# Kernel tuning notes

Hardware: AMD Instinct MI355X
Metric: run time of the kernel (lower is better)

## Reference

```python
import jax, jax.numpy as jnp
import numpy as np
import math

H, Dh, S = 8, 64, 3          # heads, dim per head, samples factor
B, T, N, K = 2, 12, 512, 16  # batch, time, nodes, local-adj width
F = H * Dh                   # features = 512
SN = int(S * math.log2(N))   # Sampled_Nodes = 27
EPS = 1e-5


def setup_inputs() -> dict:
    key = jax.random.key(0)
    ks = jax.random.split(key, 22)
    sc = 1.0 / math.sqrt(F)
    W = lambda k: jax.random.normal(k, (F, F), jnp.float32) * sc
    bb = lambda k: jax.random.normal(k, (F,), jnp.float32) * 0.01
    return {
        "x": jax.random.normal(ks[0], (B, T, N, F), jnp.float32),
        "spa_eigvalue": jax.random.normal(ks[1], (F,), jnp.float32) * 0.1,
        "spa_eigvec": jax.random.normal(ks[2], (N, F), jnp.float32) * 0.1,
        "tem_eigvalue": jax.random.normal(ks[3], (F,), jnp.float32) * 0.1,
        "tem_eigvec": jax.random.normal(ks[4], (N, F), jnp.float32) * 0.1,
        "localadj": jax.random.randint(ks[5], (N, K), 0, N),
        "Wq": W(ks[6]), "bq": bb(ks[7]),
        "Wk": W(ks[8]), "bk": bb(ks[9]),
        "Wv": W(ks[10]), "bv": bb(ks[11]),
        "Wo": W(ks[12]), "bo": bb(ks[13]),
        "w_proj": jax.random.normal(ks[14], (K,), jnp.float32) / math.sqrt(K),
        "b_proj": jax.random.normal(ks[15], (), jnp.float32) * 0.01,
        "gamma": jnp.ones((F,), jnp.float32),
        "beta": jnp.zeros((F,), jnp.float32),
        "W1": W(ks[16]), "b1": bb(ks[17]),
        "W2": W(ks[18]), "b2": bb(ks[19]),
    }


def _lin(v, Wm, bv):  # torch nn.Linear: y = x @ W^T + b, W is [out, in]
    return jnp.einsum('...i,oi->...o', v, Wm) + bv


def _ln(v, g=None, b=None):  # LayerNorm over last dim, eps=1e-5
    mu = jnp.mean(v, -1, keepdims=True)
    var = jnp.var(v, -1, keepdims=True)
    y = (v - mu) * jax.lax.rsqrt(var + EPS)
    return y * g + b if g is not None else y


def reference(x, spa_eigvalue, spa_eigvec, tem_eigvalue, tem_eigvec, localadj,
              Wq, bq, Wk, bk, Wv, bv, Wo, bo, w_proj, b_proj,
              gamma, beta, W1, b1, W2, b2):
    # eigvec @ diag(eigval) == row-wise scaling
    x_ = x + (spa_eigvec * spa_eigvalue + tem_eigvec * tem_eigvalue)
    to_heads = lambda v: v.reshape(B, T, N, H, Dh).transpose(3, 0, 1, 2, 4)  # [H,B,T,N,Dh]
    Qh = to_heads(_lin(x_, Wq, bq))
    Kh = to_heads(_lin(x_, Wk, bk))
    Vh = to_heads(_lin(x_, Wv, bv))
    # local-adjacency K sampling: [H,B,T,N,K,Dh]
    Ks = Kh[:, :, :, localadj, :]
    qks = jnp.einsum('hbtnd,hbtnkd->hbtnk', Qh, Ks)
    # importance score per query node via learned projection over K neighbors
    M = jnp.einsum('hbtnk,k->hbtn', qks, w_proj) + b_proj
    _, m_top = jax.lax.top_k(M, SN)                              # [H,B,T,SN]
    Qr = jnp.take_along_axis(Qh, m_top[..., None], axis=3)       # [H,B,T,SN,Dh]
    scores = jnp.einsum('hbtsd,hbtnd->hbtsn', Qr, Kh) / math.sqrt(Dh)
    attn = jax.nn.softmax(scores, axis=-1)                       # [H,B,T,SN,N]
    cp = jnp.argmax(attn, axis=-2)                               # best sampled query per key node [H,B,T,N]
    val = jnp.einsum('hbtsn,hbtnd->hbtsd', attn, Vh)             # [H,B,T,SN,Dh]
    out = jnp.take_along_axis(val, cp[..., None], axis=3)        # [H,B,T,N,Dh]
    out = out.transpose(1, 2, 3, 0, 4).reshape(B, T, N, F)       # merge heads
    v = _ln(_lin(out, Wo, bo), gamma, beta)
    h = jax.nn.relu(_lin(v, W1, b1))
    h = _lin(h, W2, b2) + v
    return _ln(h)
```

## Files before the change

kernel.cpp:

```cpp
#include <hip/hip_runtime.h>
#include <math.h>

#define H_    8
#define DH    64
#define NN    512
#define KADJ  16
#define FF    512
#define BTOT  24
#define ROWS  12288
#define SN_   27
#define EPS_  1e-5f

typedef short short8 __attribute__((ext_vector_type(8)));
typedef float f32x4  __attribute__((ext_vector_type(4)));

__device__ __forceinline__ ushort f2bf(float x) {
    uint u = __float_as_uint(x);
    u += 0x7FFFu + ((u >> 16) & 1u);
    return (ushort)(u >> 16);
}
__device__ __forceinline__ float bf2f(ushort h) {
    return __uint_as_float(((uint)h) << 16);
}

__device__ __forceinline__ void gload_lds16(const ushort* g, ushort* l) {
    __builtin_amdgcn_global_load_lds(
        (const __attribute__((address_space(1))) unsigned int*)g,
        (__attribute__((address_space(3))) unsigned int*)l,
        16, 0, 0);
}

__global__ __launch_bounds__(256) void add_pos_bf16(
    const float* __restrict__ x,
    const float* __restrict__ spa_val, const float* __restrict__ spa_vec,
    const float* __restrict__ tem_val, const float* __restrict__ tem_vec,
    ushort* __restrict__ xh, ushort* __restrict__ xl)
{
    int i = blockIdx.x * 256 + threadIdx.x;
    int f4  = i & 127;
    int row = i >> 7;
    int n   = row & (NN - 1);

    float4 xv = reinterpret_cast<const float4*>(x)[i];
    float4 sv = reinterpret_cast<const float4*>(spa_vec)[n * 128 + f4];
    float4 tv = reinterpret_cast<const float4*>(tem_vec)[n * 128 + f4];
    float4 se = reinterpret_cast<const float4*>(spa_val)[f4];
    float4 te = reinterpret_cast<const float4*>(tem_val)[f4];
    float r0 = xv.x + sv.x * se.x + tv.x * te.x;
    float r1 = xv.y + sv.y * se.y + tv.y * te.y;
    float r2 = xv.z + sv.z * se.z + tv.z * te.z;
    float r3 = xv.w + sv.w * se.w + tv.w * te.w;
    ushort h0 = f2bf(r0), h1 = f2bf(r1), h2 = f2bf(r2), h3 = f2bf(r3);
    reinterpret_cast<ushort4*>(xh)[i] = make_ushort4(h0, h1, h2, h3);
    reinterpret_cast<ushort4*>(xl)[i] = make_ushort4(
        f2bf(r0 - bf2f(h0)), f2bf(r1 - bf2f(h1)),
        f2bf(r2 - bf2f(h2)), f2bf(r3 - bf2f(h3)));
}

__global__ __launch_bounds__(256) void wconv_kernel(
    const float* __restrict__ w0, const float* __restrict__ w1,
    const float* __restrict__ w2, const float* __restrict__ w3,
    const float* __restrict__ w4, const float* __restrict__ w5,
    ushort* __restrict__ whi, ushort* __restrict__ wlo)
{
    const int wi = blockIdx.y;
    const float* W = wi == 0 ? w0 : wi == 1 ? w1 : wi == 2 ? w2 :
                     wi == 3 ? w3 : wi == 4 ? w4 : w5;
    int i = blockIdx.x * 256 + threadIdx.x;
    float4 v = reinterpret_cast<const float4*>(W)[i];
    ushort h0 = f2bf(v.x), h1 = f2bf(v.y), h2 = f2bf(v.z), h3 = f2bf(v.w);
    reinterpret_cast<ushort4*>(whi + (size_t)wi * 262144)[i] =
        make_ushort4(h0, h1, h2, h3);
    if (wi < 2) {
        reinterpret_cast<ushort4*>(wlo + (size_t)wi * 262144)[i] =
            make_ushort4(f2bf(v.x - bf2f(h0)), f2bf(v.y - bf2f(h1)),
                         f2bf(v.z - bf2f(h2)), f2bf(v.w - bf2f(h3)));
    }
}

#define GBM 64
#define GBN 128

__global__ __launch_bounds__(256, 2) void gemm_qk(
    const ushort* __restrict__ Axh, long aLo,
    const ushort* __restrict__ Wh0, long wLo, long wK,
    const float* __restrict__ bq, const float* __restrict__ bk,
    ushort* __restrict__ Qh, ushort* __restrict__ Ql,
    ushort* __restrict__ Kh, ushort* __restrict__ Kl)
{
    __shared__ ushort sAh[GBM * 64];
    __shared__ ushort sAl[GBM * 64];
    __shared__ ushort sBh[2][GBN * 64];
    __shared__ ushort sBl[2][GBN * 64];

    const int nx  = gridDim.x >> 3;
    const int bid = blockIdx.x;
    const int lt  = (bid & 7) * nx + (bid >> 3);
    const int rowBase = (lt >> 2) * GBM;
    const int colBase = (lt & 3) * GBN;

    const int tid  = threadIdx.x;
    const int lane = tid & 63;
    const int wid  = tid >> 6;
    const int q    = lane >> 4;
    const int fr   = lane & 15;
    const int wm   = wid & 1;
    const int wn   = wid >> 1;

    const ushort* asrc[2];
    const ushort* bsrc[4];
    #pragma unroll
    for (int c = 0; c < 2; ++c) {
        const int p   = wid * 2048 + c * 1024 + lane * 16;
        const int row = p >> 7;
        const int ss  = ((p >> 4) & 7) ^ (row & 7);
        asrc[c] = Axh + (size_t)(rowBase + row) * FF + ss * 8;
    }
    #pragma unroll
    for (int c = 0; c < 4; ++c) {
        const int p   = wid * 4096 + c * 1024 + lane * 16;
        const int row = p >> 7;
        const int ss  = ((p >> 4) & 7) ^ (row & 7);
        bsrc[c] = Wh0 + (size_t)(colBase + row) * FF + ss * 8;
    }

    f32x4 accQ[2][4], accK[2][4];
    #pragma unroll
    for (int mi = 0; mi < 2; ++mi)
        #pragma unroll
        for (int ni = 0; ni < 4; ++ni) {
            accQ[mi][ni] = (f32x4){0.f, 0.f, 0.f, 0.f};
            accK[mi][ni] = (f32x4){0.f, 0.f, 0.f, 0.f};
        }

    const int swz = fr & 7;

    for (int step = 0; step < 8; ++step) {
        #pragma unroll
        for (int c = 0; c < 2; ++c) {
            gload_lds16(asrc[c],       &sAh[wid * 1024 + c * 512]);
            gload_lds16(asrc[c] + aLo, &sAl[wid * 1024 + c * 512]);
            asrc[c] += 64;
        }
        #pragma unroll
        for (int c = 0; c < 4; ++c) {
            gload_lds16(bsrc[c],            &sBh[0][wid * 2048 + c * 512]);
            gload_lds16(bsrc[c] + wLo,      &sBl[0][wid * 2048 + c * 512]);
            gload_lds16(bsrc[c] + wK,       &sBh[1][wid * 2048 + c * 512]);
            gload_lds16(bsrc[c] + wK + wLo, &sBl[1][wid * 2048 + c * 512]);
            bsrc[c] += 64;
        }
        __syncthreads();

        #pragma unroll
        for (int ksub = 0; ksub < 2; ++ksub) {
            const int kq = (ksub * 4 + q) ^ swz;
            short8 ah[2], al[2];
            #pragma unroll
            for (int mi = 0; mi < 2; ++mi) {
                ah[mi] = *(const short8*)&sAh[(wm * 32 + mi * 16 + fr) * 64 + (kq << 3)];
                al[mi] = *(const short8*)&sAl[(wm * 32 + mi * 16 + fr) * 64 + (kq << 3)];
            }
            __builtin_amdgcn_s_setprio(1);
            #pragma unroll
            for (int qk = 0; qk < 2; ++qk) {
                short8 bh[4], bl[4];
                #pragma unroll
                for (int ni = 0; ni < 4; ++ni) {
                    bh[ni] = *(const short8*)&sBh[qk][(wn * 64 + ni * 16 + fr) * 64 + (kq << 3)];
                    bl[ni] = *(const short8*)&sBl[qk][(wn * 64 + ni * 16 + fr) * 64 + (kq << 3)];
                }
                f32x4 (*acc)[4] = qk == 0 ? accQ : accK;
                #pragma unroll
                for (int mi = 0; mi < 2; ++mi)
                    #pragma unroll
                    for (int ni = 0; ni < 4; ++ni)
                        acc[mi][ni] = __builtin_amdgcn_mfma_f32_16x16x32_bf16(
                            ah[mi], bh[ni], acc[mi][ni], 0, 0, 0);
                #pragma unroll
                for (int mi = 0; mi < 2; ++mi)
                    #pragma unroll
                    for (int ni = 0; ni < 4; ++ni)
                        acc[mi][ni] = __builtin_amdgcn_mfma_f32_16x16x32_bf16(
                            ah[mi], bl[ni], acc[mi][ni], 0, 0, 0);
                #pragma unroll
                for (int mi = 0; mi < 2; ++mi)
                    #pragma unroll
                    for (int ni = 0; ni < 4; ++ni)
                        acc[mi][ni] = __builtin_amdgcn_mfma_f32_16x16x32_bf16(
                            al[mi], bh[ni], acc[mi][ni], 0, 0, 0);
            }
            __builtin_amdgcn_s_setprio(0);
        }
        __syncthreads();
    }

    #pragma unroll
    for (int mi = 0; mi < 2; ++mi)
        #pragma unroll
        for (int ni = 0; ni < 4; ++ni) {
            const int col = colBase + wn * 64 + ni * 16 + fr;
            const float bqc = bq[col];
            const float bkc = bk[col];
            #pragma unroll
            for (int r = 0; r < 4; ++r) {
                const int row = rowBase + wm * 32 + mi * 16 + q * 4 + r;
                const size_t idx = (size_t)row * FF + col;
                float vq = accQ[mi][ni][r] + bqc;
                ushort hq = f2bf(vq);
                Qh[idx] = hq;
                Ql[idx] = f2bf(vq - bf2f(hq));
                float vk = accK[mi][ni][r] + bkc;
                ushort hk = f2bf(vk);
                Kh[idx] = hk;
                Kl[idx] = f2bf(vk - bf2f(hk));
            }
        }
}

template <int EPI, int OUT>
__global__ __launch_bounds__(256, 2) void gemm_mfma2(
    const ushort* __restrict__ Ah, const ushort* __restrict__ Wh,
    const float* __restrict__ bias, const float* __restrict__ addsrc,
    float* __restrict__ Cf, ushort* __restrict__ Cb)
{
    __shared__ ushort sA[GBM * 128];
    __shared__ ushort sB[GBN * 128];

    const int nx  = gridDim.x >> 3;
    const int bid = blockIdx.x;
    const int lt  = (bid & 7) * nx + (bid >> 3);
    const int rowBase = (lt >> 2) * GBM;
    const int colBase = (lt & 3) * GBN;

    const int tid  = threadIdx.x;
    const int lane = tid & 63;
    const int wid  = tid >> 6;
    const int q    = lane >> 4;
    const int fr   = lane & 15;
    const int wm   = wid & 1;
    const int wn   = wid >> 1;

    const ushort* asrc[4];
    const ushort* bsrc[8];
    #pragma unroll
    for (int c = 0; c < 4; ++c) {
        const int p   = wid * 4096 + c * 1024 + lane * 16;
        const int row = p >> 8;
        const int ss  = ((p >> 4) & 15) ^ (row & 7);
        asrc[c] = Ah + (size_t)(rowBase + row) * FF + ss * 8;
    }
    #pragma unroll
    for (int c = 0; c < 8; ++c) {
        const int p   = wid * 8192 + c * 1024 + lane * 16;
        const int row = p >> 8;
        const int ss  = ((p >> 4) & 15) ^ (row & 7);
        bsrc[c] = Wh + (size_t)(colBase + row) * FF + ss * 8;
    }

    f32x4 acc[2][4];
    #pragma unroll
    for (int mi = 0; mi < 2; ++mi)
        #pragma unroll
        for (int ni = 0; ni < 4; ++ni) acc[mi][ni] = (f32x4){0.f, 0.f, 0.f, 0.f};

    const int swz = fr & 7;

    for (int step = 0; step < 4; ++step) {
        #pragma unroll
        for (int c = 0; c < 4; ++c) {
            gload_lds16(asrc[c], &sA[wid * 2048 + c * 512]);
            asrc[c] += 128;
        }
        #pragma unroll
        for (int c = 0; c < 8; ++c) {
            gload_lds16(bsrc[c], &sB[wid * 4096 + c * 512]);
            bsrc[c] += 128;
        }
        __syncthreads();

        #pragma unroll
        for (int ksub = 0; ksub < 4; ++ksub) {
            const int kq = (ksub * 4 + q) ^ swz;
            short8 af[2], bf[4];
            #pragma unroll
            for (int mi = 0; mi < 2; ++mi)
                af[mi] = *(const short8*)&sA[(wm * 32 + mi * 16 + fr) * 128 + (kq << 3)];
            #pragma unroll
            for (int ni = 0; ni < 4; ++ni)
                bf[ni] = *(const short8*)&sB[(wn * 64 + ni * 16 + fr) * 128 + (kq << 3)];
            #pragma unroll
            for (int mi = 0; mi < 2; ++mi)
                #pragma unroll
                for (int ni = 0; ni < 4; ++ni)
                    acc[mi][ni] = __builtin_amdgcn_mfma_f32_16x16x32_bf16(
                        af[mi], bf[ni], acc[mi][ni], 0, 0, 0);
        }
        __syncthreads();
    }

    #pragma unroll
    for (int mi = 0; mi < 2; ++mi)
        #pragma unroll
        for (int ni = 0; ni < 4; ++ni) {
            const int col = colBase + wn * 64 + ni * 16 + fr;
            const float bcol = bias[col];
            #pragma unroll
            for (int r = 0; r < 4; ++r) {
                const int row = rowBase + wm * 32 + mi * 16 + q * 4 + r;
                float v = acc[mi][ni][r] + bcol;
                if (EPI == 1) v = fmaxf(v, 0.0f);
                if (EPI == 2) v += addsrc[(size_t)row * FF + col];
                const size_t idx = (size_t)row * FF + col;
                if (OUT == 0) Cf[idx] = v;
                if (OUT == 1) Cb[idx] = f2bf(v);
            }
        }
}

__global__ __launch_bounds__(256) void qks_M_kernel(
    const ushort* __restrict__ Qh, const ushort* __restrict__ Ql,
    const ushort* __restrict__ Kh, const ushort* __restrict__ Kl,
    const int* __restrict__ adj, const float* __restrict__ w_proj,
    const float* __restrict__ b_proj, float* __restrict__ Mout)
{
    const int unit = blockIdx.x * 16 + (threadIdx.x >> 4);
    const int l16  = threadIdx.x & 15;
    const int n    = unit & (NN - 1);
    const int hbt  = unit >> 9;
    const int h    = hbt / BTOT;
    const int bt   = hbt - h * BTOT;

    const uint headbase = (uint)(bt * NN) * FF + h * DH + l16 * 4;
    const ushort* khB = Kh + headbase;
    const ushort* klB = Kl + headbase;

    const int   aj = adj[n * KADJ + l16];
    f32x4 acc = (f32x4){0.f, 0.f, 0.f, 0.f};

    #pragma unroll
    for (int k = 0; k < KADJ; ++k) {
        const int  j   = __shfl(aj, k, 16);
        const float wk = w_proj[k];
        const uint off = (uint)j * FF;
        uint2 hu = *(const uint2*)(khB + off);
        uint2 lu = *(const uint2*)(klB + off);
        float k0 = __uint_as_float(hu.x << 16) + __uint_as_float(lu.x << 16);
        float k1 = __uint_as_float(hu.x & 0xFFFF0000u) +
                   __uint_as_float(lu.x & 0xFFFF0000u);
        float k2 = __uint_as_float(hu.y << 16) + __uint_as_float(lu.y << 16);
        float k3 = __uint_as_float(hu.y & 0xFFFF0000u) +
                   __uint_as_float(lu.y & 0xFFFF0000u);
        acc[0] += wk * k0; acc[1] += wk * k1;
        acc[2] += wk * k2; acc[3] += wk * k3;
    }

    const uint qidx = headbase + (uint)n * FF;
    uint2 qhu = *(const uint2*)(Qh + qidx);
    uint2 qlu = *(const uint2*)(Ql + qidx);
    float q0 = __uint_as_float(qhu.x << 16) + __uint_as_float(qlu.x << 16);
    float q1 = __uint_as_float(qhu.x & 0xFFFF0000u) +
               __uint_as_float(qlu.x & 0xFFFF0000u);
    float q2 = __uint_as_float(qhu.y << 16) + __uint_as_float(qlu.y << 16);
    float q3 = __uint_as_float(qhu.y & 0xFFFF0000u) +
               __uint_as_float(qlu.y & 0xFFFF0000u);
    float t = q0 * acc[0] + q1 * acc[1] + q2 * acc[2] + q3 * acc[3];
    #pragma unroll
    for (int o = 1; o <= 8; o <<= 1) t += __shfl_xor(t, o);
    if (l16 == 0) Mout[unit] = t + b_proj[0];
}

__global__ __launch_bounds__(512) void topk_kernel(
    const float* __restrict__ M, int* __restrict__ mtop)
{
    __shared__ float vals[NN];
    const int g = blockIdx.x;
    const int n = threadIdx.x;
    const float m = M[(size_t)g * NN + n];
    vals[n] = m;
    __syncthreads();

    int cnt = 0;
    #pragma unroll 16
    for (int j = 0; j < NN; ++j) {
        const float vj = vals[j];
        cnt += (vj > m || (vj == m && j < n)) ? 1 : 0;
    }
    if (cnt < SN_) mtop[g * SN_ + cnt] = n;
}

__global__ __launch_bounds__(1024) void fused_attn(
    const ushort* __restrict__ Qh, const ushort* __restrict__ Ql,
    const ushort* __restrict__ Kh, const ushort* __restrict__ Kl,
    const ushort* __restrict__ Vb, const int* __restrict__ mtop,
    ushort* __restrict__ attnout)
{
    __shared__ ushort P_lds[32 * 512];
    __shared__ ushort Vt_lds[64 * 512];
    __shared__ float red0[16][32];
    __shared__ float red1[16][32];
    __shared__ float val2[2][32][68];
    __shared__ int   cp_lds[NN];
    __shared__ int   mt[32];

    const int g = blockIdx.x;
    const int h = g / BTOT, bt = g % BTOT;
    const int tid = threadIdx.x;
    const int wave = tid >> 6, lane = tid & 63;
    const int q = lane >> 4, c = lane & 15;
    const size_t base_bt = (size_t)bt * NN * FF;
    const int hcol = h * DH;

    if (tid < 32) mt[tid] = mtop[g * SN_ + (tid < SN_ ? tid : 0)];
    __syncthreads();

    const int n0 = wave * 32;
    short8 bfh[2][2], bfl[2][2];
    #pragma unroll
    for (int nt = 0; nt < 2; ++nt) {
        const size_t kp = base_bt + (size_t)(n0 + nt * 16 + c) * FF + hcol + q * 8;
        #pragma unroll
        for (int ks = 0; ks < 2; ++ks) {
            bfh[nt][ks] = *(const short8*)&Kh[kp + ks * 32];
            bfl[nt][ks] = *(const short8*)&Kl[kp + ks * 32];
        }
    }

    ushort4 vreg[2][4];
    #pragma unroll
    for (int i = 0; i < 2; ++i) {
        const int u  = tid + i * 1024;
        const int d4 = u & 15, ng = u >> 4;
        #pragma unroll
        for (int ii = 0; ii < 4; ++ii)
            vreg[i][ii] = *(const ushort4*)&Vb[base_bt +
                (size_t)(ng * 4 + ii) * FF + hcol + d4 * 4];
    }

    short8 afh[2][2], afl[2][2];
    #pragma unroll
    for (int m = 0; m < 2; ++m) {
        const int grow = mt[m * 16 + c];
        const size_t qp = base_bt + (size_t)grow * FF + hcol + q * 8;
        #pragma unroll
        for (int ks = 0; ks < 2; ++ks) {
            afh[m][ks] = *(const short8*)&Qh[qp + ks * 32];
            afl[m][ks] = *(const short8*)&Ql[qp + ks * 32];
        }
    }

    f32x4 sc[2][2];
    #pragma unroll
    for (int m = 0; m < 2; ++m)
        #pragma unroll
        for (int nt = 0; nt < 2; ++nt) sc[m][nt] = (f32x4){0.f, 0.f, 0.f, 0.f};
    __builtin_amdgcn_s_setprio(1);
    #pragma unroll
    for (int ks = 0; ks < 2; ++ks)
        #pragma unroll
        for (int m = 0; m < 2; ++m)
            #pragma unroll
            for (int nt = 0; nt < 2; ++nt) {
                sc[m][nt] = __builtin_amdgcn_mfma_f32_16x16x32_bf16(
                    afh[m][ks], bfh[nt][ks], sc[m][nt], 0, 0, 0);
                sc[m][nt] = __builtin_amdgcn_mfma_f32_16x16x32_bf16(
                    afh[m][ks], bfl[nt][ks], sc[m][nt], 0, 0, 0);
                sc[m][nt] = __builtin_amdgcn_mfma_f32_16x16x32_bf16(
                    afl[m][ks], bfh[nt][ks], sc[m][nt], 0, 0, 0);
            }
    __builtin_amdgcn_s_setprio(0);
    #pragma unroll
    for (int m = 0; m < 2; ++m)
        #pragma unroll
        for (int nt = 0; nt < 2; ++nt)
            #pragma unroll
            for (int r = 0; r < 4; ++r) sc[m][nt][r] *= 0.125f;

    float rmax[2][4];
    #pragma unroll
    for (int m = 0; m < 2; ++m)
        #pragma unroll
        for (int r = 0; r < 4; ++r)
            rmax[m][r] = fmaxf(sc[m][0][r], sc[m][1][r]);
    #pragma unroll
    for (int off = 1; off <= 8; off <<= 1)
        #pragma unroll
        for (int m = 0; m < 2; ++m)
            #pragma unroll
            for (int r = 0; r < 4; ++r)
                rmax[m][r] = fmaxf(rmax[m][r], __shfl_xor(rmax[m][r], off));
    if (c == 0) {
        #pragma unroll
        for (int m = 0; m < 2; ++m)
            #pragma unroll
            for (int r = 0; r < 4; ++r)
                red0[wave][m * 16 + q * 4 + r] = rmax[m][r];
    }
    __syncthreads();
    float gmax[2][4];
    #pragma unroll
    for (int m = 0; m < 2; ++m)
        #pragma unroll
        for (int r = 0; r < 4; ++r) {
            const int row = m * 16 + q * 4 + r;
            float v = red0[0][row];
            #pragma unroll
            for (int w = 1; w < 16; ++w) v = fmaxf(v, red0[w][row]);
            gmax[m][r] = v;
        }

    float rsum[2][4] = {};
    #pragma unroll
    for (int m = 0; m < 2; ++m)
        #pragma unroll
        for (int nt = 0; nt < 2; ++nt)
            #pragma unroll
            for (int r = 0; r < 4; ++r) {
                float e = expf(sc[m][nt][r] - gmax[m][r]);
                sc[m][nt][r] = e;
                rsum[m][r] += e;
            }
    #pragma unroll
    for (int off = 1; off <= 8; off <<= 1)
        #pragma unroll
        for (int m = 0; m < 2; ++m)
            #pragma unroll
            for (int r = 0; r < 4; ++r)
                rsum[m][r] += __shfl_xor(rsum[m][r], off);
    if (c == 0) {
        #pragma unroll
        for (int m = 0; m < 2; ++m)
            #pragma unroll
            for (int r = 0; r < 4; ++r)
                red1[wave][m * 16 + q * 4 + r] = rsum[m][r];
    }
    __syncthreads();
    #pragma unroll
    for (int m = 0; m < 2; ++m)
        #pragma unroll
        for (int r = 0; r < 4; ++r) {
            const int row = m * 16 + q * 4 + r;
            float s = red1[0][row];
            #pragma unroll
            for (int w = 1; w < 16; ++w) s += red1[w][row];
            const float inv = 1.0f / s;
            #pragma unroll
            for (int nt = 0; nt < 2; ++nt) sc[m][nt][r] *= inv;
        }

    #pragma unroll
    for (int nt = 0; nt < 2; ++nt) {
        float bv = -INFINITY;
        int bi = 1 << 30;
        #pragma unroll
        for (int m = 0; m < 2; ++m)
            #pragma unroll
            for (int r = 0; r < 4; ++r) {
                const int row = m * 16 + q * 4 + r;
                if (row < SN_) {
                    float v = sc[m][nt][r];
                    if (v > bv) { bv = v; bi = row; }
                }
            }
        #pragma unroll
        for (int off = 16; off <= 32; off <<= 1) {
            float ov = __shfl_xor(bv, off);
            int   oi = __shfl_xor(bi, off);
            if (ov > bv || (ov == bv && oi < bi)) { bv = ov; bi = oi; }
        }
        if (q == 0) cp_lds[n0 + nt * 16 + c] = bi;
    }

    #pragma unroll
    for (int m = 0; m < 2; ++m)
        #pragma unroll
        for (int nt = 0; nt < 2; ++nt)
            #pragma unroll
            for (int r = 0; r < 4; ++r) {
                const int row = m * 16 + q * 4 + r;
                const int col = n0 + nt * 16 + c;
                P_lds[(row * 512 + col) ^ ((row & 7) << 3)] = f2bf(sc[m][nt][r]);
            }

    #pragma unroll
    for (int i = 0; i < 2; ++i) {
        const int u  = tid + i * 1024;
        const int d4 = u & 15, ng = u >> 4;
        const int n0v = ng * 4;
        #pragma unroll
        for (int j = 0; j < 4; ++j) {
            const int d = d4 * 4 + j;
            ushort4 t;
            t.x = ((const ushort*)&vreg[i][0])[j];
            t.y = ((const ushort*)&vreg[i][1])[j];
            t.z = ((const ushort*)&vreg[i][2])[j];
            t.w = ((const ushort*)&vreg[i][3])[j];
            *(ushort4*)&Vt_lds[(d * 512 + n0v) ^ ((d & 7) << 3)] = t;
        }
    }
    __syncthreads();

    const int kh = wave >> 3, rem = wave & 7;
    const int msel = rem >> 2, dt = rem & 3;
    const int dcol = dt * 16 + c;
    const int prow = msel * 16 + c;
    const int pswz = (prow & 7) << 3;
    const int vswz = (dcol & 7) << 3;
    f32x4 acc = (f32x4){0.f, 0.f, 0.f, 0.f};
    __builtin_amdgcn_s_setprio(1);
    #pragma unroll
    for (int ks8 = 0; ks8 < 8; ++ks8) {
        const int kstep = kh * 8 + ks8;
        short8 a = *(const short8*)&P_lds[(prow * 512 + kstep * 32 + q * 8) ^ pswz];
        short8 b = *(const short8*)&Vt_lds[(dcol * 512 + kstep * 32 + q * 8) ^ vswz];
        acc = __builtin_amdgcn_mfma_f32_16x16x32_bf16(a, b, acc, 0, 0, 0);
    }
    __builtin_amdgcn_s_setprio(0);
    #pragma unroll
    for (int r = 0; r < 4; ++r)
        val2[kh][msel * 16 + q * 4 + r][dt * 16 + c] = acc[r];
    __syncthreads();

    #pragma unroll
    for (int pass = 0; pass < 4; ++pass) {
        const int n  = pass * 128 + (tid >> 3);
        const int s  = cp_lds[n];
        const int d0 = (tid & 7) * 8;
        float vr[8];
        #pragma unroll
        for (int j = 0; j < 8; ++j)
            vr[j] = val2[0][s][d0 + j] + val2[1][s][d0 + j];
        uint4 u;
        u.x = (uint)f2bf(vr[0]) | ((uint)f2bf(vr[1]) << 16);
        u.y = (uint)f2bf(vr[2]) | ((uint)f2bf(vr[3]) << 16);
        u.z = (uint)f2bf(vr[4]) | ((uint)f2bf(vr[5]) << 16);
        u.w = (uint)f2bf(vr[6]) | ((uint)f2bf(vr[7]) << 16);
        *(uint4*)(attnout + base_bt + (size_t)n * FF + hcol + d0) = u;
    }
}

template <int AFFINE, int BFOUT>
__global__ __launch_bounds__(256) void ln_kernel(
    const float* __restrict__ X, const float* __restrict__ g,
    const float* __restrict__ b, float* __restrict__ Yf,
    ushort* __restrict__ Yb, int rows)
{
    const int row = blockIdx.x * 4 + (threadIdx.x >> 6);
    if (row >= rows) return;
    const int lane = threadIdx.x & 63;
    const float4* x4 = reinterpret_cast<const float4*>(X + (size_t)row * FF);
    float4 a = x4[lane];
    float4 c = x4[lane + 64];
    float s = a.x + a.y + a.z + a.w + c.x + c.y + c.z + c.w;
    float q = a.x * a.x + a.y * a.y + a.z * a.z + a.w * a.w +
              c.x * c.x + c.y * c.y + c.z * c.z + c.w * c.w;
    #pragma unroll
    for (int o = 32; o; o >>= 1) {
        s += __shfl_xor(s, o);
        q += __shfl_xor(q, o);
    }
    const float mu   = s * (1.0f / FF);
    const float var  = q * (1.0f / FF) - mu * mu;
    const float rstd = 1.0f / sqrtf(var + EPS_);

    float4 ya, yc;
    ya.x = (a.x - mu) * rstd; ya.y = (a.y - mu) * rstd;
    ya.z = (a.z - mu) * rstd; ya.w = (a.w - mu) * rstd;
    yc.x = (c.x - mu) * rstd; yc.y = (c.y - mu) * rstd;
    yc.z = (c.z - mu) * rstd; yc.w = (c.w - mu) * rstd;
    if (AFFINE) {
        float4 ga = reinterpret_cast<const float4*>(g)[lane];
        float4 gc = reinterpret_cast<const float4*>(g)[lane + 64];
        float4 ba = reinterpret_cast<const float4*>(b)[lane];
        float4 bc = reinterpret_cast<const float4*>(b)[lane + 64];
        ya.x = ya.x * ga.x + ba.x; ya.y = ya.y * ga.y + ba.y;
        ya.z = ya.z * ga.z + ba.z; ya.w = ya.w * ga.w + ba.w;
        yc.x = yc.x * gc.x + bc.x; yc.y = yc.y * gc.y + bc.y;
        yc.z = yc.z * gc.z + bc.z; yc.w = yc.w * gc.w + bc.w;
    }
    float4* y4 = reinterpret_cast<float4*>(Yf + (size_t)row * FF);
    y4[lane]      = ya;
    y4[lane + 64] = yc;
    if (BFOUT) {
        ushort4* yb = reinterpret_cast<ushort4*>(Yb + (size_t)row * FF);
        yb[lane] = make_ushort4(f2bf(ya.x), f2bf(ya.y), f2bf(ya.z), f2bf(ya.w));
        yb[lane + 64] = make_ushort4(f2bf(yc.x), f2bf(yc.y), f2bf(yc.z), f2bf(yc.w));
    }
}

extern "C" void kernel_launch(void* const* d_in, const int* in_sizes, int n_in,
                              void* d_out, int out_size, void* d_ws, size_t ws_size,
                              hipStream_t stream)
{
    const float* x       = (const float*)d_in[0];
    const float* spa_val = (const float*)d_in[1];
    const float* spa_vec = (const float*)d_in[2];
    const float* tem_val = (const float*)d_in[3];
    const float* tem_vec = (const float*)d_in[4];
    const int*   adj     = (const int*)  d_in[5];
    const float* Wq = (const float*)d_in[6];  const float* bq = (const float*)d_in[7];
    const float* Wk = (const float*)d_in[8];  const float* bk = (const float*)d_in[9];
    const float* Wv = (const float*)d_in[10]; const float* bv = (const float*)d_in[11];
    const float* Wo = (const float*)d_in[12]; const float* bo = (const float*)d_in[13];
    const float* w_proj = (const float*)d_in[14];
    const float* b_proj = (const float*)d_in[15];
    const float* gamma  = (const float*)d_in[16];
    const float* beta   = (const float*)d_in[17];
    const float* W1 = (const float*)d_in[18]; const float* b1 = (const float*)d_in[19];
    const float* W2 = (const float*)d_in[20]; const float* b2 = (const float*)d_in[21];

    float* out = (float*)d_out;

    const size_t R = (size_t)ROWS * FF;

    ushort* ws_u = (ushort*)d_ws;
    ushort* bufQh = ws_u;
    ushort* bufQl = ws_u + R;
    ushort* bufKh = ws_u + 2 * R;
    ushort* bufKl = ws_u + 3 * R;
    ushort* bufVb = ws_u + 4 * R;
    ushort* whi   = ws_u + 5 * R;
    ushort* wlo   = whi + 6 * 262144;
    float*  Mbuf  = (float*)(wlo + 2 * 262144);
    int*    mtop  = (int*)(Mbuf + (size_t)H_ * BTOT * NN);

    float* o_f32 = (float*)bufQh;
    float* v_f32 = (float*)bufKh;
    float* h2_f32 = (float*)bufQh;

    ushort* xh  = (ushort*)d_out;
    ushort* xl  = xh + R;
    ushort* attnout = xh;
    ushort* vbf = xl;
    ushort* h1b = xh;

    add_pos_bf16<<<(ROWS * FF / 4) / 256, 256, 0, stream>>>(
        x, spa_val, spa_vec, tem_val, tem_vec, xh, xl);

    wconv_kernel<<<dim3(256, 6), 256, 0, stream>>>(Wq, Wk, Wv, Wo, W1, W2, whi, wlo);

    const int NG = (ROWS / GBM) * (FF / GBN);
    gemm_qk<<<NG, 256, 0, stream>>>(xh, (long)R,
                                    whi, (long)(6 * 262144), (long)262144,
                                    bq, bk, bufQh, bufQl, bufKh, bufKl);
    gemm_mfma2<0, 1><<<NG, 256, 0, stream>>>(xh, whi + 2 * 262144, bv, nullptr,
                                             nullptr, bufVb);

    qks_M_kernel<<<(H_ * BTOT * NN) / 16, 256, 0, stream>>>(
        bufQh, bufQl, bufKh, bufKl, adj, w_proj, b_proj, Mbuf);
    topk_kernel<<<H_ * BTOT, 512, 0, stream>>>(Mbuf, mtop);

    fused_attn<<<H_ * BTOT, 1024, 0, stream>>>(
        bufQh, bufQl, bufKh, bufKl, bufVb, mtop, attnout);

    gemm_mfma2<0, 0><<<NG, 256, 0, stream>>>(attnout, whi + 3 * 262144, bo, nullptr,
                                             o_f32, nullptr);
    ln_kernel<1, 1><<<ROWS / 4, 256, 0, stream>>>(o_f32, gamma, beta, v_f32, vbf, ROWS);
    gemm_mfma2<1, 1><<<NG, 256, 0, stream>>>(vbf, whi + 4 * 262144, b1, nullptr,
                                             nullptr, h1b);
    gemm_mfma2<2, 0><<<NG, 256, 0, stream>>>(h1b, whi + 5 * 262144, b2, v_f32,
                                             h2_f32, nullptr);
    ln_kernel<0, 0><<<ROWS / 4, 256, 0, stream>>>(h2_f32, nullptr, nullptr, out, nullptr, ROWS);
}
```

Before: 211.7 us.

## Store post-attention intermediates in bf16 and drop setprio in QK GEMM

```diff
diff --git a/kernel.cpp b/kernel.cpp
--- a/kernel.cpp
+++ b/kernel.cpp
@@ -161,7 +161,6 @@
                 ah[mi] = *(const short8*)&sAh[(wm * 32 + mi * 16 + fr) * 64 + (kq << 3)];
                 al[mi] = *(const short8*)&sAl[(wm * 32 + mi * 16 + fr) * 64 + (kq << 3)];
             }
-            __builtin_amdgcn_s_setprio(1);
             #pragma unroll
             for (int qk = 0; qk < 2; ++qk) {
                 short8 bh[4], bl[4];
@@ -190,7 +189,6 @@
                         acc[mi][ni] = __builtin_amdgcn_mfma_f32_16x16x32_bf16(
                             al[mi], bh[ni], acc[mi][ni], 0, 0, 0);
             }
-            __builtin_amdgcn_s_setprio(0);
         }
         __syncthreads();
     }
@@ -221,7 +219,7 @@
 template <int EPI, int OUT>
 __global__ __launch_bounds__(256, 2) void gemm_mfma2(
     const ushort* __restrict__ Ah, const ushort* __restrict__ Wh,
-    const float* __restrict__ bias, const float* __restrict__ addsrc,
+    const float* __restrict__ bias, const ushort* __restrict__ addsrc_bf,
     float* __restrict__ Cf, ushort* __restrict__ Cb)
 {
     __shared__ ushort sA[GBM * 128];
@@ -310,8 +308,8 @@
                 const int row = rowBase + wm * 32 + mi * 16 + q * 4 + r;
                 float v = acc[mi][ni][r] + bcol;
                 if (EPI == 1) v = fmaxf(v, 0.0f);
-                if (EPI == 2) v += addsrc[(size_t)row * FF + col];
                 const size_t idx = (size_t)row * FF + col;
+                if (EPI == 2) v += bf2f(addsrc_bf[idx]);
                 if (OUT == 0) Cf[idx] = v;
                 if (OUT == 1) Cb[idx] = f2bf(v);
             }
@@ -639,52 +637,58 @@
     }
 }
 
-template <int AFFINE, int BFOUT>
-__global__ __launch_bounds__(256) void ln_kernel(
-    const float* __restrict__ X, const float* __restrict__ g,
+template <int AFFINE, int OUTF32>
+__global__ __launch_bounds__(256) void ln_bf_kernel(
+    const ushort* __restrict__ X, const float* __restrict__ g,
     const float* __restrict__ b, float* __restrict__ Yf,
     ushort* __restrict__ Yb, int rows)
 {
     const int row = blockIdx.x * 4 + (threadIdx.x >> 6);
     if (row >= rows) return;
     const int lane = threadIdx.x & 63;
-    const float4* x4 = reinterpret_cast<const float4*>(X + (size_t)row * FF);
-    float4 a = x4[lane];
-    float4 c = x4[lane + 64];
-    float s = a.x + a.y + a.z + a.w + c.x + c.y + c.z + c.w;
-    float q = a.x * a.x + a.y * a.y + a.z * a.z + a.w * a.w +
-              c.x * c.x + c.y * c.y + c.z * c.z + c.w * c.w;
+
+    ushort4 u0 = *(const ushort4*)&X[(size_t)row * FF + lane * 8];
+    ushort4 u1 = *(const ushort4*)&X[(size_t)row * FF + lane * 8 + 4];
+    float f[8];
+    f[0] = bf2f(u0.x); f[1] = bf2f(u0.y); f[2] = bf2f(u0.z); f[3] = bf2f(u0.w);
+    f[4] = bf2f(u1.x); f[5] = bf2f(u1.y); f[6] = bf2f(u1.z); f[7] = bf2f(u1.w);
+
+    float s = 0.f, qq = 0.f;
+    #pragma unroll
+    for (int j = 0; j < 8; ++j) { s += f[j]; qq += f[j] * f[j]; }
     #pragma unroll
     for (int o = 32; o; o >>= 1) {
-        s += __shfl_xor(s, o);
-        q += __shfl_xor(q, o);
+        s  += __shfl_xor(s, o);
+        qq += __shfl_xor(qq, o);
     }
     const float mu   = s * (1.0f / FF);
-    const float var  = q * (1.0f / FF) - mu * mu;
+    const float var  = qq * (1.0f / FF) - mu * mu;
     const float rstd = 1.0f / sqrtf(var + EPS_);
 
-    float4 ya, yc;
-    ya.x = (a.x - mu) * rstd; ya.y = (a.y - mu) * rstd;
-    ya.z = (a.z - mu) * rstd; ya.w = (a.w - mu) * rstd;
-    yc.x = (c.x - mu) * rstd; yc.y = (c.y - mu) * rstd;
-    yc.z = (c.z - mu) * rstd; yc.w = (c.w - mu) * rstd;
+    float y[8];
+    #pragma unroll
+    for (int j = 0; j < 8; ++j) y[j] = (f[j] - mu) * rstd;
     if (AFFINE) {
-        float4 ga = reinterpret_cast<const float4*>(g)[lane];
-        float4 gc = reinterpret_cast<const float4*>(g)[lane + 64];
-        float4 ba = reinterpret_cast<const float4*>(b)[lane];
-        float4 bc = reinterpret_cast<const float4*>(b)[lane + 64];
-        ya.x = ya.x * ga.x + ba.x; ya.y = ya.y * ga.y + ba.y;
-        ya.z = ya.z * ga.z + ba.z; ya.w = ya.w * ga.w + ba.w;
-        yc.x = yc.x * gc.x + bc.x; yc.y = yc.y * gc.y + bc.y;
-        yc.z = yc.z * gc.z + bc.z; yc.w = yc.w * gc.w + bc.w;
-    }
-    float4* y4 = reinterpret_cast<float4*>(Yf + (size_t)row * FF);
-    y4[lane]      = ya;
-    y4[lane + 64] = yc;
-    if (BFOUT) {
-        ushort4* yb = reinterpret_cast<ushort4*>(Yb + (size_t)row * FF);
-        yb[lane] = make_ushort4(f2bf(ya.x), f2bf(ya.y), f2bf(ya.z), f2bf(ya.w));
-        yb[lane + 64] = make_ushort4(f2bf(yc.x), f2bf(yc.y), f2bf(yc.z), f2bf(yc.w));
+        float4 ga = *(const float4*)&g[lane * 8];
+        float4 gb = *(const float4*)&g[lane * 8 + 4];
+        float4 ba = *(const float4*)&b[lane * 8];
+        float4 bb = *(const float4*)&b[lane * 8 + 4];
+        y[0] = y[0] * ga.x + ba.x; y[1] = y[1] * ga.y + ba.y;
+        y[2] = y[2] * ga.z + ba.z; y[3] = y[3] * ga.w + ba.w;
+        y[4] = y[4] * gb.x + bb.x; y[5] = y[5] * gb.y + bb.y;
+        y[6] = y[6] * gb.z + bb.z; y[7] = y[7] * gb.w + bb.w;
+    }
+    if (OUTF32) {
+        float4* yo = (float4*)&Yf[(size_t)row * FF + lane * 8];
+        yo[0] = make_float4(y[0], y[1], y[2], y[3]);
+        yo[1] = make_float4(y[4], y[5], y[6], y[7]);
+    } else {
+        uint4 u;
+        u.x = (uint)f2bf(y[0]) | ((uint)f2bf(y[1]) << 16);
+        u.y = (uint)f2bf(y[2]) | ((uint)f2bf(y[3]) << 16);
+        u.z = (uint)f2bf(y[4]) | ((uint)f2bf(y[5]) << 16);
+        u.w = (uint)f2bf(y[6]) | ((uint)f2bf(y[7]) << 16);
+        *(uint4*)&Yb[(size_t)row * FF + lane * 8] = u;
     }
 }
 
@@ -724,9 +728,8 @@
     float*  Mbuf  = (float*)(wlo + 2 * 262144);
     int*    mtop  = (int*)(Mbuf + (size_t)H_ * BTOT * NN);
 
-    float* o_f32 = (float*)bufQh;
-    float* v_f32 = (float*)bufKh;
-    float* h2_f32 = (float*)bufQh;
+    ushort* o_bf  = bufQh;
+    ushort* h2_bf = bufKh;
 
     ushort* xh  = (ushort*)d_out;
     ushort* xl  = xh + R;
@@ -753,12 +756,14 @@
     fused_attn<<<H_ * BTOT, 1024, 0, stream>>>(
         bufQh, bufQl, bufKh, bufKl, bufVb, mtop, attnout);
 
-    gemm_mfma2<0, 0><<<NG, 256, 0, stream>>>(attnout, whi + 3 * 262144, bo, nullptr,
-                                             o_f32, nullptr);
-    ln_kernel<1, 1><<<ROWS / 4, 256, 0, stream>>>(o_f32, gamma, beta, v_f32, vbf, ROWS);
+    gemm_mfma2<0, 1><<<NG, 256, 0, stream>>>(attnout, whi + 3 * 262144, bo, nullptr,
+                                             nullptr, o_bf);
+    ln_bf_kernel<1, 0><<<ROWS / 4, 256, 0, stream>>>(o_bf, gamma, beta,
+                                                     nullptr, vbf, ROWS);
     gemm_mfma2<1, 1><<<NG, 256, 0, stream>>>(vbf, whi + 4 * 262144, b1, nullptr,
                                              nullptr, h1b);
-    gemm_mfma2<2, 0><<<NG, 256, 0, stream>>>(h1b, whi + 5 * 262144, b2, v_f32,
-                                             h2_f32, nullptr);
-    ln_kernel<0, 0><<<ROWS / 4, 256, 0, stream>>>(h2_f32, nullptr, nullptr, out, nullptr, ROWS);
-}
+    gemm_mfma2<2, 1><<<NG, 256, 0, stream>>>(h1b, whi + 5 * 262144, b2, vbf,
+                                             nullptr, h2_bf);
+    ln_bf_kernel<0, 1><<<ROWS / 4, 256, 0, stream>>>(h2_bf, nullptr, nullptr,
+                                                     out, nullptr, ROWS);
+}
```

Result: faster. 206.9 us (median of 2 runs) (-2.3%).
